# Kernel tuning notes

Hardware: AMD Instinct MI355X
Metric: run time of the kernel (lower is better)

The kernel has to match this reference:

```python
import jax, jax.numpy as jnp
import numpy as np

C_IN, C, N_HEAD = 256, 32, 8

def setup_inputs() -> dict:
    key = jax.random.key(0)
    ks = jax.random.split(key, 9)
    B, S = 4, 2048
    x = jax.random.normal(ks[0], (B, S, C_IN), dtype=jnp.float32)
    bias = jax.random.normal(ks[1], (1, N_HEAD, S, S), dtype=jnp.float32)
    s = 0.02
    Wq = jax.random.normal(ks[2], (C_IN, C * N_HEAD), dtype=jnp.float32) * s
    Wk = jax.random.normal(ks[3], (C_IN, C * N_HEAD), dtype=jnp.float32) * s
    Wv = jax.random.normal(ks[4], (C_IN, C * N_HEAD), dtype=jnp.float32) * s
    Wg = jax.random.normal(ks[5], (C_IN, C * N_HEAD), dtype=jnp.float32) * s
    bg = jnp.zeros((C * N_HEAD,), dtype=jnp.float32)
    Wo = jax.random.normal(ks[6], (C * N_HEAD, C_IN), dtype=jnp.float32) * s
    bo = jnp.zeros((C_IN,), dtype=jnp.float32)
    return {"x": x, "bias": bias, "Wq": Wq, "Wk": Wk, "Wv": Wv,
            "Wg": Wg, "bg": bg, "Wo": Wo, "bo": bo}

def reference(x, bias, Wq, Wk, Wv, Wg, bg, Wo, bo):
    B, S, _ = x.shape
    # projections (attn_dim = -2, so no movedim needed for [B, S, c_in])
    q = (x @ Wq).reshape(B, S, N_HEAD, C).transpose(0, 2, 1, 3)  # [B,H,S,C]
    k = (x @ Wk).reshape(B, S, N_HEAD, C).transpose(0, 2, 1, 3)
    v = (x @ Wv).reshape(B, S, N_HEAD, C).transpose(0, 2, 1, 3)
    q = q / jnp.sqrt(jnp.asarray(C, dtype=q.dtype))
    a = jnp.einsum('bhqc,bhkc->bhqk', q, k) + bias  # [B,H,S,S]
    a = jax.nn.softmax(a, axis=-1)
    o = jnp.einsum('bhqk,bhkc->bhqc', a, v)         # [B,H,S,C]
    o = o.transpose(0, 2, 1, 3).reshape(B, S, N_HEAD * C)
    g = jax.nn.sigmoid(x @ Wg + bg)
    o = g * o
    return o @ Wo + bo
```

## Files before the change

kernel.cpp:

```cpp
#include <hip/hip_runtime.h>

#define BB   4
#define SS   2048
#define HH   8
#define CC   32
#define CIN  256

typedef unsigned short u16;
typedef unsigned int   u32;
typedef u16 u16x4 __attribute__((ext_vector_type(4)));
typedef u16 u16x8 __attribute__((ext_vector_type(8)));
typedef __bf16 bf16x8 __attribute__((ext_vector_type(8)));
typedef float f32x4 __attribute__((ext_vector_type(4)));


__device__ __forceinline__ f32x4 mfma16(u16x8 a, u16x8 b, f32x4 c) {
  return __builtin_amdgcn_mfma_f32_16x16x32_bf16(
      __builtin_bit_cast(bf16x8, a), __builtin_bit_cast(bf16x8, b), c, 0, 0, 0);
}

__device__ __forceinline__ u32 cvtpk(float a, float b) {
  u32 r;
  asm("v_cvt_pk_bf16_f32 %0, %1, %2" : "=v"(r) : "v"(a), "v"(b));
  return r;
}

__device__ __forceinline__ f32x4 ldf4(const float* p) {
  float4 v = *(const float4*)p;
  f32x4 z = {v.x, v.y, v.z, v.w};
  return z;
}

__device__ __forceinline__ u16 bf16_rne(float x) {
  unsigned u = __float_as_uint(x);
  u += 0x7FFFu + ((u >> 16) & 1u);
  return (u16)(u >> 16);
}
__device__ __forceinline__ void cvt_pair(float x, u16 &hi, u16 &lo) {
  hi = bf16_rne(x);
  lo = bf16_rne(x - __uint_as_float(((unsigned)hi) << 16));
}

__global__ void k_cvt_x(const float* __restrict__ x,
                        u16* __restrict__ xh, u16* __restrict__ xl) {
  int i = (blockIdx.x * 256 + threadIdx.x) * 4;
  float4 v = *(const float4*)(x + i);
  u16x4 h, l;
  u16 th, tl;
  cvt_pair(v.x, th, tl); h[0] = th; l[0] = tl;
  cvt_pair(v.y, th, tl); h[1] = th; l[1] = tl;
  cvt_pair(v.z, th, tl); h[2] = th; l[2] = tl;
  cvt_pair(v.w, th, tl); h[3] = th; l[3] = tl;
  *(u16x4*)(xh + i) = h;
  *(u16x4*)(xl + i) = l;
}

__global__ void k_cvt_w(const float* __restrict__ Wq, const float* __restrict__ Wk,
                        const float* __restrict__ Wv, const float* __restrict__ Wg,
                        const float* __restrict__ Wo,
                        u16* __restrict__ wt4h, u16* __restrict__ wt4l,
                        u16* __restrict__ woth, u16* __restrict__ wotl) {
  __shared__ float tile[64][65];
  const int mat = blockIdx.x / 16, tt = blockIdx.x % 16;
  const int m0 = (tt >> 2) * 64, n0 = (tt & 3) * 64;
  const float* W = (mat == 0) ? Wq : (mat == 1) ? Wk : (mat == 2) ? Wv
                 : (mat == 3) ? Wg : Wo;
  const int tr = threadIdx.x >> 6;
  const int tc = threadIdx.x & 63;
#pragma unroll
  for (int i = 0; i < 16; ++i) {
    int row = i * 4 + tr;
    tile[row][tc] = W[(m0 + row) * 256 + n0 + tc];
  }
  __syncthreads();
  u16* dh = (mat < 4) ? wt4h : woth;
  u16* dl = (mat < 4) ? wt4l : wotl;
  const int nbase = (mat < 4) ? mat * 256 : 0;
#pragma unroll
  for (int i = 0; i < 16; ++i) {
    int row = i * 4 + tr;
    u16 hi, lo; cvt_pair(tile[tc][row], hi, lo);
    dh[(nbase + n0 + row) * 256 + m0 + tc] = hi;
    dl[(nbase + n0 + row) * 256 + m0 + tc] = lo;
  }
}

__global__ __launch_bounds__(256, 2) void k_proj(
    const u16* __restrict__ xh, const u16* __restrict__ xl,
    const u16* __restrict__ wt4h, const u16* __restrict__ wt4l,
    const float* __restrict__ bg,
    u16* __restrict__ qh, u16* __restrict__ ql,
    u16* __restrict__ kh, u16* __restrict__ kl,
    u16* __restrict__ vth, u16* __restrict__ vtl,
    float* __restrict__ g) {
  const int m0 = blockIdx.x * 128;
  const int n0 = blockIdx.y * 128;
  const int wave = threadIdx.x >> 6;
  const int lane = threadIdx.x & 63;
  const int wm = (wave >> 1) * 64, wn = (wave & 1) * 64;
  const int l15 = lane & 15, lg = lane >> 4;

  f32x4 acc[4][4] = {};
  for (int ks = 0; ks < 8; ++ks) {
    u16x8 a_h[4], a_l[4], b_h[4], b_l[4];
#pragma unroll
    for (int mt = 0; mt < 4; ++mt) {
      int base = (m0 + wm + mt * 16 + l15) * 256 + ks * 32 + lg * 8;
      a_h[mt] = *(const u16x8*)(xh + base);
      a_l[mt] = *(const u16x8*)(xl + base);
    }
#pragma unroll
    for (int nt = 0; nt < 4; ++nt) {
      int base = (n0 + wn + nt * 16 + l15) * 256 + ks * 32 + lg * 8;
      b_h[nt] = *(const u16x8*)(wt4h + base);
      b_l[nt] = *(const u16x8*)(wt4l + base);
    }
#pragma unroll
    for (int mt = 0; mt < 4; ++mt)
#pragma unroll
      for (int nt = 0; nt < 4; ++nt) {
        acc[mt][nt] = mfma16(a_h[mt], b_h[nt], acc[mt][nt]);
        acc[mt][nt] = mfma16(a_h[mt], b_l[nt], acc[mt][nt]);
        acc[mt][nt] = mfma16(a_l[mt], b_h[nt], acc[mt][nt]);
      }
  }

  const float qscale = 0.17677669529663687f;
#pragma unroll
  for (int mt = 0; mt < 4; ++mt)
#pragma unroll
    for (int nt = 0; nt < 4; ++nt) {
      const int rowb = m0 + wm + mt * 16 + lg * 4;
      const int col  = n0 + wn + nt * 16 + l15;
      const int bb = rowb >> 11, s = rowb & 2047;
      const int mid = col >> 8, d = col & 255;
      const int hh = d >> 5, c = d & 31;
      if (mid == 3) {
#pragma unroll
        for (int r = 0; r < 4; ++r) {
          float gv = 1.0f / (1.0f + __expf(-(acc[mt][nt][r] + bg[d])));
          g[(rowb + r) * 256 + d] = gv;
        }
      } else if (mid == 2) {
        u16x4 vh4, vl4;
#pragma unroll
        for (int r = 0; r < 4; ++r) {
          u16 th, tl; cvt_pair(acc[mt][nt][r], th, tl);
          vh4[r] = th; vl4[r] = tl;
        }
        size_t idx = ((size_t)(bb * HH + hh) * CC + c) * SS + s;
        *(u16x4*)(vth + idx) = vh4;
        *(u16x4*)(vtl + idx) = vl4;
      } else {
#pragma unroll
        for (int r = 0; r < 4; ++r) {
          float val = acc[mt][nt][r];
          if (mid == 0) val *= qscale;
          u16 th, tl; cvt_pair(val, th, tl);
          size_t idx = ((size_t)(bb * HH + hh) * SS + s + r) * CC + c;
          if (mid == 0) { qh[idx] = th; ql[idx] = tl; }
          else          { kh[idx] = th; kl[idx] = tl; }
        }
      }
    }
}

__global__ __launch_bounds__(256, 2) void k_attn(
    const u16* __restrict__ qh, const u16* __restrict__ ql,
    const u16* __restrict__ kh, const u16* __restrict__ kl,
    const u16* __restrict__ vth, const u16* __restrict__ vtl,
    const float* __restrict__ bias,
    float* __restrict__ n0, float* __restrict__ n1,
    float* __restrict__ d0, float* __restrict__ d1) {
  __shared__ __align__(16) u32 lds32[19968];
  u16* ldsu = (u16*)lds32;

  const int idx = blockIdx.x;
  const int h   = idx & 7;
  const int js  = (idx >> 3) & 1;
  const int bp  = (idx >> 4) & 1;
  const int q0  = (idx >> 5) * 128;
  const int w    = threadIdx.x >> 6;
  const int lane = threadIdx.x & 63;
  const int l15 = lane & 15, lg = lane >> 4;
  const int t = threadIdx.x;
  const int jbase = js * 1024;

  float* nbuf = js ? n1 : n0;
  float* dbuf = js ? d1 : d0;

  const int kj = t >> 2, kc = (t & 3) * 8;
  const int vc = t >> 3, vj = (t & 7) * 8;
  size_t kb[2], vb[2];
#pragma unroll
  for (int b2 = 0; b2 < 2; ++b2) {
    const int bh2 = (bp * 2 + b2) * HH + h;
    kb[b2] = ((size_t)bh2 * SS + jbase + kj) * CC + kc;
    vb[b2] = ((size_t)bh2 * CC + vc) * SS + jbase + vj;
  }

  u16x8 qfh[2][2], qfl[2][2];
#pragma unroll
  for (int b2 = 0; b2 < 2; ++b2)
#pragma unroll
    for (int qt = 0; qt < 2; ++qt) {
      int base = (((bp * 2 + b2) * HH + h) * SS + q0 + w * 32 + qt * 16 + l15)
                 * CC + lg * 8;
      qfh[b2][qt] = *(const u16x8*)(qh + base);
      qfl[b2][qt] = *(const u16x8*)(ql + base);
    }

  const float* biasQ[2];
#pragma unroll
  for (int qt = 0; qt < 2; ++qt)
    biasQ[qt] = bias + (size_t)h * SS * SS
              + (size_t)(q0 + w * 32 + qt * 16 + l15) * SS + jbase + lg * 4;

  u32* pw = lds32 + 10752 + w * 2304;

  f32x4 oacc[2][2][2] = {};
  float rs[2][2] = {};

  f32x4 bcur[2][4];
  {
    u16x8 a = *(const u16x8*)(kh + kb[0]);
    u16x8 c = *(const u16x8*)(kl + kb[0]);
    u16x8 e = *(const u16x8*)(vth + vb[0]);
    u16x8 f = *(const u16x8*)(vtl + vb[0]);
#pragma unroll
    for (int qt = 0; qt < 2; ++qt)
#pragma unroll
      for (int at = 0; at < 4; ++at)
        bcur[qt][at] = ldf4(biasQ[qt] + at * 16);
    *(u16x8*)(ldsu + kj * 40 + kc) = a;
    *(u16x8*)(ldsu + 2560 + kj * 40 + kc) = c;
    *(u16x8*)(ldsu + 5120 + vc * 88 + vj) = e;
    *(u16x8*)(ldsu + 7936 + vc * 88 + vj) = f;
  }
  __syncthreads();

#pragma unroll 1
  for (int jt = 0; jt < 16; ++jt) {
#pragma unroll
    for (int b2 = 0; b2 < 2; ++b2) {
      const u16* lk = ldsu + b2 * 10752;
      u16* ln = ldsu + (b2 ^ 1) * 10752;
      const bool hasNext = (b2 == 0) || (jt < 15);
      const int njt = (b2 == 0) ? jt : jt + 1;
      const int nb2 = b2 ^ 1;

      u16x8 skh, skl, svh, svl;
      if (hasNext) {
        size_t gk = kb[nb2] + (size_t)njt * 64 * CC;
        size_t gv = vb[nb2] + (size_t)njt * 64;
        skh = *(const u16x8*)(kh + gk);
        skl = *(const u16x8*)(kl + gk);
        svh = *(const u16x8*)(vth + gv);
        svl = *(const u16x8*)(vtl + gv);
      }
      f32x4 bnxt[2][4];
      if (b2 == 1 && jt < 15) {
#pragma unroll
        for (int qt = 0; qt < 2; ++qt)
#pragma unroll
          for (int at = 0; at < 4; ++at)
            bnxt[qt][at] = ldf4(biasQ[qt] + (jt + 1) * 64 + at * 16);
      }

      u16x8 ka_h[4], ka_l[4];
#pragma unroll
      for (int at = 0; at < 4; ++at) {
        int base = (at * 16 + l15) * 40 + lg * 8;
        ka_h[at] = *(const u16x8*)(lk + base);
        ka_l[at] = *(const u16x8*)(lk + 2560 + base);
      }
      f32x4 sacc[2][4];
#pragma unroll
      for (int qt = 0; qt < 2; ++qt)
#pragma unroll
        for (int at = 0; at < 4; ++at)
          sacc[qt][at] = bcur[qt][at];
#pragma unroll
      for (int at = 0; at < 4; ++at)
#pragma unroll
        for (int qt = 0; qt < 2; ++qt) {
          sacc[qt][at] = mfma16(ka_h[at], qfh[b2][qt], sacc[qt][at]);
          sacc[qt][at] = mfma16(ka_h[at], qfl[b2][qt], sacc[qt][at]);
          sacc[qt][at] = mfma16(ka_l[at], qfh[b2][qt], sacc[qt][at]);
        }
#pragma unroll
      for (int qt = 0; qt < 2; ++qt) {
        u32* pq = pw + qt * 1152;
#pragma unroll
        for (int at = 0; at < 4; ++at) {
          float p0 = __expf(sacc[qt][at][0]);
          float p1 = __expf(sacc[qt][at][1]);
          float p2 = __expf(sacc[qt][at][2]);
          float p3 = __expf(sacc[qt][at][3]);
          rs[b2][qt] += (p0 + p1) + (p2 + p3);
          u32 hA = cvtpk(p0, p1), hB = cvtpk(p2, p3);
          float f0 = __uint_as_float(hA << 16);
          float f1 = __uint_as_float(hA & 0xffff0000u);
          float f2 = __uint_as_float(hB << 16);
          float f3 = __uint_as_float(hB & 0xffff0000u);
          u32 lA = cvtpk(p0 - f0, p1 - f1);
          u32 lB = cvtpk(p2 - f2, p3 - f3);
          int off = l15 * 36 + 8 * at + 2 * lg;
          uint2 Hv; Hv.x = hA; Hv.y = hB;
          uint2 Lv; Lv.x = lA; Lv.y = lB;
          *(uint2*)&pq[off] = Hv;
          *(uint2*)&pq[off + 576] = Lv;
        }
      }
#pragma unroll
      for (int ks = 0; ks < 2; ++ks) {
        int roff = l15 * 36 + 16 * ks + 4 * lg;
        u16x8 pa_h[2], pa_l[2];
#pragma unroll
        for (int qt = 0; qt < 2; ++qt) {
          pa_h[qt] = *(const u16x8*)(pw + qt * 1152 + roff);
          pa_l[qt] = *(const u16x8*)(pw + qt * 1152 + 576 + roff);
        }
#pragma unroll
        for (int ct = 0; ct < 2; ++ct) {
          int voff = (ct * 16 + l15) * 88 + ks * 32 + lg * 8;
          u16x8 vfh = *(const u16x8*)(lk + 5120 + voff);
          u16x8 vfl = *(const u16x8*)(lk + 7936 + voff);
#pragma unroll
          for (int qt = 0; qt < 2; ++qt) {
            oacc[b2][qt][ct] = mfma16(pa_h[qt], vfh, oacc[b2][qt][ct]);
            oacc[b2][qt][ct] = mfma16(pa_h[qt], vfl, oacc[b2][qt][ct]);
            oacc[b2][qt][ct] = mfma16(pa_l[qt], vfh, oacc[b2][qt][ct]);
          }
        }
      }
      if (hasNext) {
        *(u16x8*)(ln + kj * 40 + kc) = skh;
        *(u16x8*)(ln + 2560 + kj * 40 + kc) = skl;
        *(u16x8*)(ln + 5120 + vc * 88 + vj) = svh;
        *(u16x8*)(ln + 7936 + vc * 88 + vj) = svl;
      }
      if (b2 == 1 && jt < 15) {
#pragma unroll
        for (int qt = 0; qt < 2; ++qt)
#pragma unroll
          for (int at = 0; at < 4; ++at)
            bcur[qt][at] = bnxt[qt][at];
      }
      __syncthreads();
    }
  }

#pragma unroll
  for (int b2 = 0; b2 < 2; ++b2) {
    const int bfull = bp * 2 + b2;
#pragma unroll
    for (int qt = 0; qt < 2; ++qt) {
      rs[b2][qt] += __shfl_xor(rs[b2][qt], 16, 64);
      rs[b2][qt] += __shfl_xor(rs[b2][qt], 32, 64);
      if (lg == 0)
        dbuf[(size_t)(bfull * SS + q0 + w * 32 + qt * 16 + l15) * HH + h] =
            rs[b2][qt];
#pragma unroll
      for (int ct = 0; ct < 2; ++ct)
#pragma unroll
        for (int r = 0; r < 4; ++r) {
          int qg = q0 + w * 32 + qt * 16 + lg * 4 + r;
          nbuf[((size_t)(bfull * SS + qg) * HH + h) * CC + ct * 16 + l15] =
              oacc[b2][qt][ct][r];
        }
    }
  }
}

__global__ __launch_bounds__(256, 2) void k_out(
    const float* __restrict__ n0, const float* __restrict__ n1,
    const float* __restrict__ d0, const float* __restrict__ d1,
    const float* __restrict__ g,
    const u16* __restrict__ woth, const u16* __restrict__ wotl,
    const float* __restrict__ bo, float* __restrict__ out) {
  const int m0 = blockIdx.x * 32;
  const int nn0 = blockIdx.y * 128;
  const int wave = threadIdx.x >> 6;
  const int lane = threadIdx.x & 63;
  const int wn = wave * 32;
  const int l15 = lane & 15, lg = lane >> 4;

  f32x4 acc[2][2] = {};
  for (int ks = 0; ks < 8; ++ks) {
    u16x8 a_h[2], a_l[2], b_h[2], b_l[2];
#pragma unroll
    for (int mt = 0; mt < 2; ++mt) {
      int row = m0 + mt * 16 + l15;
      int base = row * 256 + ks * 32 + lg * 8;
      float inv = 1.0f / (d0[row * 8 + ks] + d1[row * 8 + ks]);
      float4 a0 = *(const float4*)(n0 + base);
      float4 a1 = *(const float4*)(n0 + base + 4);
      float4 c0 = *(const float4*)(n1 + base);
      float4 c1 = *(const float4*)(n1 + base + 4);
      float4 g0 = *(const float4*)(g + base);
      float4 g1 = *(const float4*)(g + base + 4);
      float pr[8] = {(a0.x + c0.x) * inv * g0.x, (a0.y + c0.y) * inv * g0.y,
                     (a0.z + c0.z) * inv * g0.z, (a0.w + c0.w) * inv * g0.w,
                     (a1.x + c1.x) * inv * g1.x, (a1.y + c1.y) * inv * g1.y,
                     (a1.z + c1.z) * inv * g1.z, (a1.w + c1.w) * inv * g1.w};
      union { u16 s[8]; u16x8 v; } uh, ul;
#pragma unroll
      for (int e = 0; e < 8; ++e) { u16 th, tl; cvt_pair(pr[e], th, tl); uh.s[e] = th; ul.s[e] = tl; }
      a_h[mt] = uh.v; a_l[mt] = ul.v;
    }
#pragma unroll
    for (int nt = 0; nt < 2; ++nt) {
      int base = (nn0 + wn + nt * 16 + l15) * 256 + ks * 32 + lg * 8;
      b_h[nt] = *(const u16x8*)(woth + base);
      b_l[nt] = *(const u16x8*)(wotl + base);
    }
#pragma unroll
    for (int mt = 0; mt < 2; ++mt)
#pragma unroll
      for (int nt = 0; nt < 2; ++nt) {
        acc[mt][nt] = mfma16(a_h[mt], b_h[nt], acc[mt][nt]);
        acc[mt][nt] = mfma16(a_h[mt], b_l[nt], acc[mt][nt]);
        acc[mt][nt] = mfma16(a_l[mt], b_h[nt], acc[mt][nt]);
      }
  }
#pragma unroll
  for (int mt = 0; mt < 2; ++mt)
#pragma unroll
    for (int nt = 0; nt < 2; ++nt)
#pragma unroll
      for (int r = 0; r < 4; ++r) {
        int row = m0 + mt * 16 + lg * 4 + r;
        int col = nn0 + wn + nt * 16 + l15;
        out[row * 256 + col] = acc[mt][nt][r] + bo[col];
      }
}

extern "C" void kernel_launch(void* const* d_in, const int* in_sizes, int n_in,
                              void* d_out, int out_size, void* d_ws, size_t ws_size,
                              hipStream_t stream) {
  const float* x    = (const float*)d_in[0];
  const float* bias = (const float*)d_in[1];
  const float* Wq   = (const float*)d_in[2];
  const float* Wk   = (const float*)d_in[3];
  const float* Wv   = (const float*)d_in[4];
  const float* Wg   = (const float*)d_in[5];
  const float* bg   = (const float*)d_in[6];
  const float* Wo   = (const float*)d_in[7];
  const float* bo   = (const float*)d_in[8];
  float* out = (float*)d_out;

  char* p = (char*)d_ws;
  size_t used = 0;
  auto alloc = [&](size_t bytes) -> void* {
    void* r = p + used;
    used += (bytes + 255) & ~(size_t)255;
    return r;
  };
  const size_t NTOK = (size_t)BB * SS * CIN;
  u16* xh   = (u16*)alloc(NTOK * 2);
  u16* xl   = (u16*)alloc(NTOK * 2);
  u16* wt4h = (u16*)alloc(1024 * 256 * 2);
  u16* wt4l = (u16*)alloc(1024 * 256 * 2);
  u16* woth = (u16*)alloc(256 * 256 * 2);
  u16* wotl = (u16*)alloc(256 * 256 * 2);
  u16* qh   = (u16*)alloc(NTOK * 2);
  u16* ql   = (u16*)alloc(NTOK * 2);
  u16* kh   = (u16*)alloc(NTOK * 2);
  u16* kl   = (u16*)alloc(NTOK * 2);
  u16* vth  = (u16*)alloc(NTOK * 2);
  u16* vtl  = (u16*)alloc(NTOK * 2);
  float* gbuf = (float*)alloc(NTOK * 4);
  float* nb0  = (float*)alloc(NTOK * 4);
  float* nb1  = (float*)alloc(NTOK * 4);
  float* db0  = (float*)alloc((size_t)BB * SS * HH * 4);
  float* db1  = (float*)alloc((size_t)BB * SS * HH * 4);
  if (used > ws_size) return;

  k_cvt_x<<<dim3(2048), dim3(256), 0, stream>>>(x, xh, xl);
  k_cvt_w<<<dim3(80), dim3(256), 0, stream>>>(Wq, Wk, Wv, Wg, Wo, wt4h, wt4l, woth, wotl);
  k_proj<<<dim3(64, 8), dim3(256), 0, stream>>>(xh, xl, wt4h, wt4l, bg,
                                                qh, ql, kh, kl, vth, vtl, gbuf);
  k_attn<<<dim3(512), dim3(256), 0, stream>>>(qh, ql, kh, kl, vth, vtl, bias,
                                              nb0, nb1, db0, db1);
  k_out<<<dim3(256, 2), dim3(256), 0, stream>>>(nb0, nb1, db0, db1, gbuf,
                                                woth, wotl, bo, out);
}
```

Baseline: 166.5 us.

## Process all four batches per attention block and split keys four ways

Each attention block now covers all four batch elements for one head and query tile and handles a quarter of the key range, where before it covered two batches and half the keys. Each bias tile is therefore loaded once and reused across all four batches, halving bias traffic, which dominates memory reads. The cost is double the per-thread query fragments and accumulators, which raises register pressure, plus four partial numerator and denominator buffers that the output kernel must read and sum, adding extra global traffic.

After: 362.5 us. +117.7%, slower.

```diff
diff --git a/kernel.cpp b/kernel.cpp
--- a/kernel.cpp
+++ b/kernel.cpp
@@ -171,40 +171,41 @@
     const u16* __restrict__ vth, const u16* __restrict__ vtl,
     const float* __restrict__ bias,
     float* __restrict__ n0, float* __restrict__ n1,
-    float* __restrict__ d0, float* __restrict__ d1) {
+    float* __restrict__ n2, float* __restrict__ n3,
+    float* __restrict__ d0, float* __restrict__ d1,
+    float* __restrict__ d2, float* __restrict__ d3) {
   __shared__ __align__(16) u32 lds32[19968];
   u16* ldsu = (u16*)lds32;
 
   const int idx = blockIdx.x;
   const int h   = idx & 7;
-  const int js  = (idx >> 3) & 1;
-  const int bp  = (idx >> 4) & 1;
+  const int js  = (idx >> 3) & 3;
   const int q0  = (idx >> 5) * 128;
   const int w    = threadIdx.x >> 6;
   const int lane = threadIdx.x & 63;
   const int l15 = lane & 15, lg = lane >> 4;
   const int t = threadIdx.x;
-  const int jbase = js * 1024;
-
-  float* nbuf = js ? n1 : n0;
-  float* dbuf = js ? d1 : d0;
+  const int jbase = js * 512;
+
+  float* nbuf = (js == 0) ? n0 : (js == 1) ? n1 : (js == 2) ? n2 : n3;
+  float* dbuf = (js == 0) ? d0 : (js == 1) ? d1 : (js == 2) ? d2 : d3;
 
   const int kj = t >> 2, kc = (t & 3) * 8;
   const int vc = t >> 3, vj = (t & 7) * 8;
-  size_t kb[2], vb[2];
-#pragma unroll
-  for (int b2 = 0; b2 < 2; ++b2) {
-    const int bh2 = (bp * 2 + b2) * HH + h;
+  size_t kb[4], vb[4];
+#pragma unroll
+  for (int b2 = 0; b2 < 4; ++b2) {
+    const int bh2 = b2 * HH + h;
     kb[b2] = ((size_t)bh2 * SS + jbase + kj) * CC + kc;
     vb[b2] = ((size_t)bh2 * CC + vc) * SS + jbase + vj;
   }
 
-  u16x8 qfh[2][2], qfl[2][2];
-#pragma unroll
-  for (int b2 = 0; b2 < 2; ++b2)
+  u16x8 qfh[4][2], qfl[4][2];
+#pragma unroll
+  for (int b2 = 0; b2 < 4; ++b2)
 #pragma unroll
     for (int qt = 0; qt < 2; ++qt) {
-      int base = (((bp * 2 + b2) * HH + h) * SS + q0 + w * 32 + qt * 16 + l15)
+      int base = ((b2 * HH + h) * SS + q0 + w * 32 + qt * 16 + l15)
                  * CC + lg * 8;
       qfh[b2][qt] = *(const u16x8*)(qh + base);
       qfl[b2][qt] = *(const u16x8*)(ql + base);
@@ -218,8 +219,8 @@
 
   u32* pw = lds32 + 10752 + w * 2304;
 
-  f32x4 oacc[2][2][2] = {};
-  float rs[2][2] = {};
+  f32x4 oacc[4][2][2] = {};
+  float rs[4][2] = {};
 
   f32x4 bcur[2][4];
   {
@@ -240,14 +241,14 @@
   __syncthreads();
 
 #pragma unroll 1
-  for (int jt = 0; jt < 16; ++jt) {
-#pragma unroll
-    for (int b2 = 0; b2 < 2; ++b2) {
-      const u16* lk = ldsu + b2 * 10752;
-      u16* ln = ldsu + (b2 ^ 1) * 10752;
-      const bool hasNext = (b2 == 0) || (jt < 15);
-      const int njt = (b2 == 0) ? jt : jt + 1;
-      const int nb2 = b2 ^ 1;
+  for (int jt = 0; jt < 8; ++jt) {
+#pragma unroll
+    for (int b2 = 0; b2 < 4; ++b2) {
+      const u16* lk = ldsu + (b2 & 1) * 10752;
+      u16* ln = ldsu + ((b2 & 1) ^ 1) * 10752;
+      const bool hasNext = (b2 < 3) || (jt < 7);
+      const int njt = (b2 == 3) ? jt + 1 : jt;
+      const int nb2 = (b2 + 1) & 3;
 
       u16x8 skh, skl, svh, svl;
       if (hasNext) {
@@ -259,7 +260,7 @@
         svl = *(const u16x8*)(vtl + gv);
       }
       f32x4 bnxt[2][4];
-      if (b2 == 1 && jt < 15) {
+      if (b2 == 3 && jt < 7) {
 #pragma unroll
         for (int qt = 0; qt < 2; ++qt)
 #pragma unroll
@@ -340,7 +341,7 @@
         *(u16x8*)(ln + 5120 + vc * 88 + vj) = svh;
         *(u16x8*)(ln + 7936 + vc * 88 + vj) = svl;
       }
-      if (b2 == 1 && jt < 15) {
+      if (b2 == 3 && jt < 7) {
 #pragma unroll
         for (int qt = 0; qt < 2; ++qt)
 #pragma unroll
@@ -352,21 +353,20 @@
   }
 
 #pragma unroll
-  for (int b2 = 0; b2 < 2; ++b2) {
-    const int bfull = bp * 2 + b2;
+  for (int b2 = 0; b2 < 4; ++b2) {
 #pragma unroll
     for (int qt = 0; qt < 2; ++qt) {
       rs[b2][qt] += __shfl_xor(rs[b2][qt], 16, 64);
       rs[b2][qt] += __shfl_xor(rs[b2][qt], 32, 64);
       if (lg == 0)
-        dbuf[(size_t)(bfull * SS + q0 + w * 32 + qt * 16 + l15) * HH + h] =
+        dbuf[(size_t)(b2 * SS + q0 + w * 32 + qt * 16 + l15) * HH + h] =
             rs[b2][qt];
 #pragma unroll
       for (int ct = 0; ct < 2; ++ct)
 #pragma unroll
         for (int r = 0; r < 4; ++r) {
           int qg = q0 + w * 32 + qt * 16 + lg * 4 + r;
-          nbuf[((size_t)(bfull * SS + qg) * HH + h) * CC + ct * 16 + l15] =
+          nbuf[((size_t)(b2 * SS + qg) * HH + h) * CC + ct * 16 + l15] =
               oacc[b2][qt][ct][r];
         }
     }
@@ -375,7 +375,9 @@
 
 __global__ __launch_bounds__(256, 2) void k_out(
     const float* __restrict__ n0, const float* __restrict__ n1,
+    const float* __restrict__ n2, const float* __restrict__ n3,
     const float* __restrict__ d0, const float* __restrict__ d1,
+    const float* __restrict__ d2, const float* __restrict__ d3,
     const float* __restrict__ g,
     const u16* __restrict__ woth, const u16* __restrict__ wotl,
     const float* __restrict__ bo, float* __restrict__ out) {
@@ -393,17 +395,27 @@
     for (int mt = 0; mt < 2; ++mt) {
       int row = m0 + mt * 16 + l15;
       int base = row * 256 + ks * 32 + lg * 8;
-      float inv = 1.0f / (d0[row * 8 + ks] + d1[row * 8 + ks]);
+      float inv = 1.0f / (d0[row * 8 + ks] + d1[row * 8 + ks] +
+                          d2[row * 8 + ks] + d3[row * 8 + ks]);
       float4 a0 = *(const float4*)(n0 + base);
       float4 a1 = *(const float4*)(n0 + base + 4);
       float4 c0 = *(const float4*)(n1 + base);
       float4 c1 = *(const float4*)(n1 + base + 4);
+      float4 e0 = *(const float4*)(n2 + base);
+      float4 e1 = *(const float4*)(n2 + base + 4);
+      float4 f0 = *(const float4*)(n3 + base);
+      float4 f1 = *(const float4*)(n3 + base + 4);
       float4 g0 = *(const float4*)(g + base);
       float4 g1 = *(const float4*)(g + base + 4);
-      float pr[8] = {(a0.x + c0.x) * inv * g0.x, (a0.y + c0.y) * inv * g0.y,
-                     (a0.z + c0.z) * inv * g0.z, (a0.w + c0.w) * inv * g0.w,
-                     (a1.x + c1.x) * inv * g1.x, (a1.y + c1.y) * inv * g1.y,
-                     (a1.z + c1.z) * inv * g1.z, (a1.w + c1.w) * inv * g1.w};
+      float pr[8] = {
+        (a0.x + c0.x + e0.x + f0.x) * inv * g0.x,
+        (a0.y + c0.y + e0.y + f0.y) * inv * g0.y,
+        (a0.z + c0.z + e0.z + f0.z) * inv * g0.z,
+        (a0.w + c0.w + e0.w + f0.w) * inv * g0.w,
+        (a1.x + c1.x + e1.x + f1.x) * inv * g1.x,
+        (a1.y + c1.y + e1.y + f1.y) * inv * g1.y,
+        (a1.z + c1.z + e1.z + f1.z) * inv * g1.z,
+        (a1.w + c1.w + e1.w + f1.w) * inv * g1.w};
       union { u16 s[8]; u16x8 v; } uh, ul;
 #pragma unroll
       for (int e = 0; e < 8; ++e) { u16 th, tl; cvt_pair(pr[e], th, tl); uh.s[e] = th; ul.s[e] = tl; }
@@ -473,8 +485,12 @@
   float* gbuf = (float*)alloc(NTOK * 4);
   float* nb0  = (float*)alloc(NTOK * 4);
   float* nb1  = (float*)alloc(NTOK * 4);
+  float* nb2  = (float*)alloc(NTOK * 4);
+  float* nb3  = (float*)alloc(NTOK * 4);
   float* db0  = (float*)alloc((size_t)BB * SS * HH * 4);
   float* db1  = (float*)alloc((size_t)BB * SS * HH * 4);
+  float* db2  = (float*)alloc((size_t)BB * SS * HH * 4);
+  float* db3  = (float*)alloc((size_t)BB * SS * HH * 4);
   if (used > ws_size) return;
 
   k_cvt_x<<<dim3(2048), dim3(256), 0, stream>>>(x, xh, xl);
@@ -482,7 +498,9 @@
   k_proj<<<dim3(64, 8), dim3(256), 0, stream>>>(xh, xl, wt4h, wt4l, bg,
                                                 qh, ql, kh, kl, vth, vtl, gbuf);
   k_attn<<<dim3(512), dim3(256), 0, stream>>>(qh, ql, kh, kl, vth, vtl, bias,
-                                              nb0, nb1, db0, db1);
-  k_out<<<dim3(256, 2), dim3(256), 0, stream>>>(nb0, nb1, db0, db1, gbuf,
+                                              nb0, nb1, nb2, nb3,
+                                              db0, db1, db2, db3);
+  k_out<<<dim3(256, 2), dim3(256), 0, stream>>>(nb0, nb1, nb2, nb3,
+                                                db0, db1, db2, db3, gbuf,
                                                 woth, wotl, bo, out);
 }
```
